# Optimization experiments

Hardware: AMD Instinct MI355X
Metric: run time of the kernel (lower is better)

The kernel has to match this reference:

```python
import jax, jax.numpy as jnp
import numpy as np

EPS = 1e-5  # torch InstanceNorm2d default eps

def instance_norm(x):
    # per-sample, per-channel normalization over spatial dims (affine=False)
    m = jnp.mean(x, axis=(2, 3), keepdims=True)
    v = jnp.var(x, axis=(2, 3), keepdims=True)
    return (x - m) * jax.lax.rsqrt(v + EPS)

def conv2d(x, w, b, stride, pad):
    y = jax.lax.conv_general_dilated(
        x, w, (stride, stride), [(pad, pad), (pad, pad)],
        dimension_numbers=('NCHW', 'OIHW', 'NCHW'))
    return y + b[None, :, None, None]

def res_block(x, w1, b1, w2, b2):
    out = conv2d(jax.nn.relu(instance_norm(x)), w1, b1, 1, 1)
    out = conv2d(jax.nn.relu(instance_norm(out)), w2, b2, 1, 1)
    return out + x

def res_block_strided(x, w1, b1, w2, b2, ws, bs):
    out = conv2d(jax.nn.relu(instance_norm(x)), w1, b1, 2, 1)
    out = conv2d(jax.nn.relu(instance_norm(out)), w2, b2, 1, 1)
    return out + conv2d(x, ws, bs, 2, 0)  # 1x1 strided skip projection

def setup_inputs() -> dict:
    key = jax.random.key(0)
    ks = jax.random.split(key, 12)
    B, N, C, H, W = 64, 1, 3, 256, 256
    TEXT, EMB, F, HEADS = 256, 512, 32, 5
    FH, FW = H // 16, W // 16  # 16, 16
    def rn(k, shape, scale=0.05):
        return jax.random.normal(k, shape, dtype=jnp.float32) * scale
    z = lambda *s: jnp.zeros(s, jnp.float32)
    return {
        'x': jax.random.normal(ks[0], (B, N, C, H, W), jnp.float32),
        'text_vector': jax.random.normal(ks[1], (B, TEXT), jnp.float32),
        'conv1_w': rn(ks[2], (F, C, 7, 7)),
        'conv1_b': z(F),
        'rbs_w1': rn(ks[3], (3, F, F, 3, 3)),  # 3 strided resblocks
        'rbs_b1': z(3, F),
        'rbs_w2': rn(ks[4], (3, F, F, 3, 3)),
        'rbs_b2': z(3, F),
        'rbs_ws': rn(ks[5], (3, F, F, 1, 1)),
        'rbs_bs': z(3, F),
        'rb_w1': rn(ks[6], (2, F, F, 3, 3)),  # 2 plain resblocks
        'rb_b1': z(2, F),
        'rb_w2': rn(ks[7], (2, F, F, 3, 3)),
        'rb_b2': z(2, F),
        'attn_w': rn(ks[8], (HEADS, FH * FW, TEXT)),  # torch Linear [out,in] per head
        'attn_b': z(HEADS, FH * FW),
        'final_w': rn(ks[9], (EMB, FH * FW * HEADS)),
        'final_b': z(EMB),
    }

def reference(x, text_vector, conv1_w, conv1_b, rbs_w1, rbs_b1, rbs_w2, rbs_b2,
              rbs_ws, rbs_bs, rb_w1, rb_b1, rb_w2, rb_b2, attn_w, attn_b,
              final_w, final_b):
    B, N, C, H, W = x.shape
    feat = x.reshape(B, N * C, H, W)
    feat = instance_norm(feat)
    feat = conv2d(feat, conv1_w, conv1_b, 2, 3)
    # block1 = strided + plain; block2 = strided + plain; block3 = strided
    feat = res_block_strided(feat, rbs_w1[0], rbs_b1[0], rbs_w2[0], rbs_b2[0], rbs_ws[0], rbs_bs[0])
    feat = res_block(feat, rb_w1[0], rb_b1[0], rb_w2[0], rb_b2[0])
    feat = res_block_strided(feat, rbs_w1[1], rbs_b1[1], rbs_w2[1], rbs_b2[1], rbs_ws[1], rbs_bs[1])
    feat = res_block(feat, rb_w1[1], rb_b1[1], rb_w2[1], rb_b2[1])
    feat = res_block_strided(feat, rbs_w1[2], rbs_b1[2], rbs_w2[2], rbs_b2[2], rbs_ws[2], rbs_bs[2])
    # feat: [B, 32, FH, FW]
    HEADS = attn_w.shape[0]
    FH, FW = feat.shape[2], feat.shape[3]
    # sigmoid-gated spatial attention logits per head: [B, HEADS, FH, FW]
    a = jax.nn.sigmoid(jnp.einsum('bt,hot->bho', text_vector, attn_w) + attn_b[None])
    a = a.reshape(B, HEADS, FH, FW)
    # channel scores: spatial sum of gate * feature -> [B, HEADS, C]
    scores = jnp.einsum('bhij,bcij->bhc', a, feat)
    probs = jax.nn.softmax(scores, axis=-1)  # old F.softmax over channel dim
    # weighted channel sum -> per-head attention map [B, HEADS, FH, FW]
    amaps = jnp.einsum('bhc,bcij->bhij', probs, feat)
    out = amaps.reshape(B, -1) @ final_w.T + final_b
    return out
```

## Files before the change

kernel.cpp:

```cpp
#include <hip/hip_runtime.h>
#include <cstdint>
#include <cstddef>

#define INORM_EPS 1e-5f

typedef _Float16 f16;
typedef f16 f16x8 __attribute__((ext_vector_type(8)));
typedef f16 f16x4 __attribute__((ext_vector_type(4)));
typedef float f32x4 __attribute__((ext_vector_type(4)));

__global__ __launch_bounds__(256) void prep(
    const float* __restrict__ rbs_w1, const float* __restrict__ rbs_w2,
    const float* __restrict__ rb_w1, const float* __restrict__ rb_w2,
    const float* __restrict__ rbs_ws, const float* __restrict__ conv1_w,
    float2* __restrict__ SP, f16* __restrict__ wp3, f16* __restrict__ wp1,
    f16* __restrict__ wp7) {
  int i = blockIdx.x * 256 + threadIdx.x;
  if (i < 20672) { SP[i] = make_float2(0.f, 0.f); return; }
  i -= 20672;
  if (i < 92160) {
    int mat = i / 9216, r = i % 9216;
    int p = r >> 10, f = (r >> 9) & 1, l = (r >> 3) & 63, j = r & 7;
    int co = f * 16 + (l & 15), ci = (l >> 4) * 8 + j;
    const float* src; int m;
    if (mat < 3) { src = rbs_w1; m = mat; }
    else if (mat < 6) { src = rbs_w2; m = mat - 3; }
    else if (mat < 8) { src = rb_w1; m = mat - 6; }
    else { src = rb_w2; m = mat - 8; }
    wp3[i] = (f16)src[m * 9216 + co * 288 + ci * 9 + p];
    return;
  }
  i -= 92160;
  if (i < 3072) {
    int mat = i / 1024, r = i % 1024;
    int f = r >> 9, l = (r >> 3) & 63, j = r & 7;
    wp1[i] = (f16)rbs_ws[mat * 1024 + (f * 16 + (l & 15)) * 32 + (l >> 4) * 8 + j];
    return;
  }
  i -= 3072;
  if (i >= 7168) return;
  int ky = i >> 10, f = (i >> 9) & 1, l = (i >> 3) & 63, j = i & 7;
  int k = (l >> 4) * 8 + j, kx = k >> 2, ci = k & 3;
  float v = 0.f;
  if (kx < 7 && ci < 3) v = conv1_w[(f * 16 + (l & 15)) * 147 + ci * 49 + ky * 7 + kx];
  wp7[i] = (f16)v;
}

__global__ __launch_bounds__(256) void stats_raw(const float* __restrict__ in,
                                                 float2* __restrict__ st, int HW) {
  const int map = blockIdx.x >> 3, chunk = blockIdx.x & 7;
  const int n4 = HW >> 5;
  const float4* p = (const float4*)(in + (size_t)map * HW + (size_t)chunk * (HW >> 3));
  float s = 0.f, ss = 0.f;
  for (int i = threadIdx.x; i < n4; i += 256) {
    float4 v = p[i];
    s += v.x + v.y + v.z + v.w;
    ss += v.x * v.x + v.y * v.y + v.z * v.z + v.w * v.w;
  }
  __shared__ float r0[256], r1[256];
  r0[threadIdx.x] = s;
  r1[threadIdx.x] = ss;
  __syncthreads();
  for (int off = 128; off > 0; off >>= 1) {
    if ((int)threadIdx.x < off) {
      r0[threadIdx.x] += r0[threadIdx.x + off];
      r1[threadIdx.x] += r1[threadIdx.x + off];
    }
    __syncthreads();
  }
  if (threadIdx.x == 0) {
    atomicAdd(&st[map].x, r0[0]);
    atomicAdd(&st[map].y, r1[0]);
  }
}

__global__ __launch_bounds__(256) void packx(const float* __restrict__ x,
                                             const float2* __restrict__ SPx,
                                             f16* __restrict__ xP) {
  int u = blockIdx.x * 256 + threadIdx.x;
  if (u >= 262 * 262) return;
  int b = blockIdx.z;
  int r = u / 262, c = u % 262;
  f16x4 out;
  out[0] = (f16)0; out[1] = (f16)0; out[2] = (f16)0; out[3] = (f16)0;
  if (r >= 3 && r < 259 && c >= 3 && c < 259) {
    int ir = r - 3, ic = c - 3;
#pragma unroll
    for (int ci = 0; ci < 3; ci++) {
      float2 s = SPx[b * 3 + ci];
      float mean = s.x * (1.f / 65536.f);
      float rstd = rsqrtf(s.y * (1.f / 65536.f) - mean * mean + INORM_EPS);
      out[ci] = (f16)((x[((size_t)b * 3 + ci) * 65536 + ir * 256 + ic] - mean) * rstd);
    }
  }
  *(f16x4*)(xP + ((size_t)b * 68644 + u) * 4) = out;
}

template <int W, int SKIP>
__global__ __launch_bounds__(256) void conv3r(
    const f16* __restrict__ Rin, const float2* __restrict__ SPin, float inv_hw,
    const f16* __restrict__ wp, const float* __restrict__ bias,
    const float* __restrict__ bias2, const f16* __restrict__ skip,
    const f16* __restrict__ wps, f16* __restrict__ Rout,
    float2* __restrict__ ostats) {
  constexpr int TPR = W / 16;
  constexpr int RPB = 8;
  constexpr int LEN = (RPB * TPR) / 4;
  const int t = threadIdx.x, w = t >> 6, l = t & 63;
  const int n = l & 15, q = l >> 4;
  const int b = blockIdx.z;
  const int tx = w % TPR;
  const int y0 = blockIdx.x * RPB + (w / TPR) * LEN;
  const int x = (tx << 4) + n;
  const f16* Rb = Rin + (size_t)b * W * W * 32;

  f16x8 sc, sh;
#pragma unroll
  for (int j = 0; j < 8; j++) {
    float2 s = SPin[b * 32 + q * 8 + j];
    float mean = s.x * inv_hw;
    float rstd = rsqrtf(s.y * inv_hw - mean * mean + INORM_EPS);
    sc[j] = (f16)rstd;
    sh[j] = (f16)(-mean * rstd);
  }

  f16x8 wf[18];
#pragma unroll
  for (int i = 0; i < 18; i++) wf[i] = *(const f16x8*)(wp + i * 512 + l * 8);
  f16x8 wsf0, wsf1;
  if (SKIP == 2) {
    wsf0 = *(const f16x8*)(wps + l * 8);
    wsf1 = *(const f16x8*)(wps + 512 + l * 8);
  }
  float b0 = bias[n], b1 = bias[16 + n];
  if (SKIP == 2) { b0 += bias2[n]; b1 += bias2[16 + n]; }

  f16* ro = Rout + (size_t)b * W * W * 32;
  const f16* sb = skip ? skip + (size_t)b * (SKIP == 2 ? 4 : 1) * W * W * 32 : nullptr;

  bool okc[3];
#pragma unroll
  for (int kx = 0; kx < 3; kx++) okc[kx] = (unsigned)(x + kx - 1) < (unsigned)W;

  auto rowload = [&](int gy, f16x8* dst) {
    int gyc = min(max(gy, 0), W - 1);
#pragma unroll
    for (int kx = 0; kx < 3; kx++) {
      int gxc = min(max(x + kx - 1, 0), W - 1);
      dst[kx] = *(const f16x8*)(Rb + ((size_t)gyc * W + gxc) * 32 + q * 8);
    }
  };
  auto rownorm = [&](int gy, const f16x8* src, f16x8* dst) {
    bool okr = (unsigned)gy < (unsigned)W;
#pragma unroll
    for (int kx = 0; kx < 3; kx++) {
      f16x8 v = src[kx] * sc + sh;
#pragma unroll
      for (int e = 0; e < 8; e++) v[e] = v[e] > (f16)0 ? v[e] : (f16)0;
      f16x8 z = {};
      dst[kx] = (okr && okc[kx]) ? v : z;
    }
  };

  float sm0 = 0.f, sq0 = 0.f, sm1 = 0.f, sq1 = 0.f;
  f16x8 win[9];
  f16x8 tmp[3], pf[3];
#pragma unroll
  for (int jj = 0; jj < 3; jj++) {
    rowload(y0 + jj - 1, tmp);
    rownorm(y0 + jj - 1, tmp, &win[jj * 3]);
  }

#pragma unroll
  for (int i = 0; i < LEN; i++) {
    int y = y0 + i;
    if (i + 1 < LEN) rowload(y0 + i + 2, pf);
    f32x4 acc0 = {0.f, 0.f, 0.f, 0.f}, acc1 = {0.f, 0.f, 0.f, 0.f};
#pragma unroll
    for (int ky = 0; ky < 3; ky++) {
      int slot = (i + ky) % 3;
#pragma unroll
      for (int kx = 0; kx < 3; kx++) {
        f16x8 a = win[slot * 3 + kx];
        acc0 = __builtin_amdgcn_mfma_f32_16x16x32_f16(a, wf[2 * (ky * 3 + kx)], acc0, 0, 0, 0);
        acc1 = __builtin_amdgcn_mfma_f32_16x16x32_f16(a, wf[2 * (ky * 3 + kx) + 1], acc1, 0, 0, 0);
      }
    }
    if (SKIP == 2) {
      const int Ws = 2 * W;
      f16x8 as = *(const f16x8*)(sb + ((size_t)(2 * y) * Ws + 2 * x) * 32 + q * 8);
      acc0 = __builtin_amdgcn_mfma_f32_16x16x32_f16(as, wsf0, acc0, 0, 0, 0);
      acc1 = __builtin_amdgcn_mfma_f32_16x16x32_f16(as, wsf1, acc1, 0, 0, 0);
    }
#pragma unroll
    for (int r = 0; r < 4; r++) {
      size_t px = (size_t)y * W + (tx << 4) + q * 4 + r;
      float v0 = acc0[r] + b0;
      float v1 = acc1[r] + b1;
      if (SKIP == 1) {
        v0 += (float)sb[px * 32 + n];
        v1 += (float)sb[px * 32 + 16 + n];
      }
      ro[px * 32 + n] = (f16)v0;
      ro[px * 32 + 16 + n] = (f16)v1;
      sm0 += v0; sq0 += v0 * v0;
      sm1 += v1; sq1 += v1 * v1;
    }
    if (i + 1 < LEN) rownorm(y0 + i + 2, pf, &win[(i % 3) * 3]);
  }
  if (ostats) {
    sm0 += __shfl_xor(sm0, 16); sm0 += __shfl_xor(sm0, 32);
    sq0 += __shfl_xor(sq0, 16); sq0 += __shfl_xor(sq0, 32);
    sm1 += __shfl_xor(sm1, 16); sm1 += __shfl_xor(sm1, 32);
    sq1 += __shfl_xor(sq1, 16); sq1 += __shfl_xor(sq1, 32);
    if (l < 16) {
      atomicAdd(&ostats[b * 32 + n].x, sm0);
      atomicAdd(&ostats[b * 32 + n].y, sq0);
      atomicAdd(&ostats[b * 32 + 16 + n].x, sm1);
      atomicAdd(&ostats[b * 32 + 16 + n].y, sq1);
    }
  }
}

template <int WIN, int STRIDE, int SKIP>
__global__ __launch_bounds__(256) void conv3n(
    const f16* __restrict__ Rin, const float2* __restrict__ SPin, float inv_hw,
    const f16* __restrict__ wp, const float* __restrict__ bias,
    const float* __restrict__ bias2, const f16* __restrict__ skip,
    const f16* __restrict__ wps, f16* __restrict__ Rout,
    float2* __restrict__ ostats) {
  constexpr int WOUT = WIN / STRIDE;
  constexpr int TPR = WOUT / 16;
  constexpr int RPB = (WOUT >= 32) ? 4 : 8;
  constexpr int UNITS = TPR * RPB;
  constexpr int U = UNITS / 4;
  const int t = threadIdx.x, w = t >> 6, l = t & 63;
  const int n = l & 15, q = l >> 4;
  const int b = blockIdx.z;
  const int yb = blockIdx.x * RPB;
  const f16* Rb = Rin + (size_t)b * WIN * WIN * 32;

  f16x8 sc, sh;
#pragma unroll
  for (int j = 0; j < 8; j++) {
    float2 s = SPin[b * 32 + q * 8 + j];
    float mean = s.x * inv_hw;
    float rstd = rsqrtf(s.y * inv_hw - mean * mean + INORM_EPS);
    sc[j] = (f16)rstd;
    sh[j] = (f16)(-mean * rstd);
  }

  f16x8 wf[18];
#pragma unroll
  for (int i = 0; i < 18; i++) wf[i] = *(const f16x8*)(wp + i * 512 + l * 8);
  f16x8 wsf0, wsf1;
  if (SKIP == 2) {
    wsf0 = *(const f16x8*)(wps + l * 8);
    wsf1 = *(const f16x8*)(wps + 512 + l * 8);
  }
  float b0 = bias[n], b1 = bias[16 + n];
  if (SKIP == 2) { b0 += bias2[n]; b1 += bias2[16 + n]; }

  f16* ro = Rout + (size_t)b * WOUT * WOUT * 32;
  const f16* sb = skip ? skip + (size_t)b * (SKIP == 2 ? 4 : 1) * WOUT * WOUT * 32 : nullptr;

  auto load_u = [&](int u, f16x8* a) {
    int ty = u / TPR, tx = u % TPR;
    int y = yb + ty;
#pragma unroll
    for (int kx = 0; kx < 3; kx++) {
      int gx = STRIDE * ((tx << 4) + n) + kx - 1;
      int gxc = min(max(gx, 0), WIN - 1);
#pragma unroll
      for (int ky = 0; ky < 3; ky++) {
        int gy = STRIDE * y + ky - 1;
        int gyc = min(max(gy, 0), WIN - 1);
        a[ky * 3 + kx] = *(const f16x8*)(Rb + ((size_t)gyc * WIN + gxc) * 32 + q * 8);
      }
    }
  };
  auto norm_u = [&](int u, f16x8* a) {
    int ty = u / TPR, tx = u % TPR;
    int y = yb + ty;
#pragma unroll
    for (int kx = 0; kx < 3; kx++) {
      int gx = STRIDE * ((tx << 4) + n) + kx - 1;
      bool okx = (unsigned)gx < (unsigned)WIN;
#pragma unroll
      for (int ky = 0; ky < 3; ky++) {
        int gy = STRIDE * y + ky - 1;
        bool ok = okx && ((unsigned)gy < (unsigned)WIN);
        f16x8 v = a[ky * 3 + kx] * sc + sh;
#pragma unroll
        for (int e = 0; e < 8; e++) v[e] = v[e] > (f16)0 ? v[e] : (f16)0;
        f16x8 z = {};
        a[ky * 3 + kx] = ok ? v : z;
      }
    }
  };

  float sm0 = 0.f, sq0 = 0.f, sm1 = 0.f, sq1 = 0.f;
  f16x8 araw[9], anxt[9];
  load_u(w, araw);
#pragma unroll
  for (int i = 0; i < U; i++) {
    int u = w + 4 * i;
    if (i + 1 < U) load_u(u + 4, anxt);
    norm_u(u, araw);
    int ty = u / TPR, tx = u % TPR;
    int y = yb + ty, x0 = tx << 4;
    f32x4 acc0 = {0.f, 0.f, 0.f, 0.f}, acc1 = {0.f, 0.f, 0.f, 0.f};
#pragma unroll
    for (int p = 0; p < 9; p++) {
      acc0 = __builtin_amdgcn_mfma_f32_16x16x32_f16(araw[p], wf[2 * p], acc0, 0, 0, 0);
      acc1 = __builtin_amdgcn_mfma_f32_16x16x32_f16(araw[p], wf[2 * p + 1], acc1, 0, 0, 0);
    }
    if (SKIP == 2) {
      const int Ws = 2 * WOUT;
      f16x8 as = *(const f16x8*)(sb + ((size_t)(2 * y) * Ws + 2 * (x0 + n)) * 32 + q * 8);
      acc0 = __builtin_amdgcn_mfma_f32_16x16x32_f16(as, wsf0, acc0, 0, 0, 0);
      acc1 = __builtin_amdgcn_mfma_f32_16x16x32_f16(as, wsf1, acc1, 0, 0, 0);
    }
#pragma unroll
    for (int r = 0; r < 4; r++) {
      size_t px = (size_t)y * WOUT + x0 + q * 4 + r;
      float v0 = acc0[r] + b0;
      float v1 = acc1[r] + b1;
      if (SKIP == 1) {
        v0 += (float)sb[px * 32 + n];
        v1 += (float)sb[px * 32 + 16 + n];
      }
      ro[px * 32 + n] = (f16)v0;
      ro[px * 32 + 16 + n] = (f16)v1;
      sm0 += v0; sq0 += v0 * v0;
      sm1 += v1; sq1 += v1 * v1;
    }
#pragma unroll
    for (int p = 0; p < 9; p++) araw[p] = anxt[p];
  }
  if (ostats) {
    sm0 += __shfl_xor(sm0, 16); sm0 += __shfl_xor(sm0, 32);
    sq0 += __shfl_xor(sq0, 16); sq0 += __shfl_xor(sq0, 32);
    sm1 += __shfl_xor(sm1, 16); sm1 += __shfl_xor(sm1, 32);
    sq1 += __shfl_xor(sq1, 16); sq1 += __shfl_xor(sq1, 32);
    if (l < 16) {
      atomicAdd(&ostats[b * 32 + n].x, sm0);
      atomicAdd(&ostats[b * 32 + n].y, sq0);
      atomicAdd(&ostats[b * 32 + 16 + n].x, sm1);
      atomicAdd(&ostats[b * 32 + 16 + n].y, sq1);
    }
  }
}

__global__ __launch_bounds__(256) void conv7(
    const f16* __restrict__ xP, const f16* __restrict__ wp,
    const float* __restrict__ bias, f16* __restrict__ Rout,
    float2* __restrict__ ostats) {
  const int t = threadIdx.x, w = t >> 6, l = t & 63;
  const int n = l & 15, q = l >> 4;
  const int b = blockIdx.z;
  const int yb = blockIdx.x * 8;
  const f16* Xb = xP + (size_t)b * 68644 * 4;
  f16x8 wf[14];
#pragma unroll
  for (int i = 0; i < 14; i++) wf[i] = *(const f16x8*)(wp + i * 512 + l * 8);
  float b0 = bias[n], b1 = bias[16 + n];
  float sm0 = 0.f, sq0 = 0.f, sm1 = 0.f, sq1 = 0.f;
  f16* ro = Rout + (size_t)b * 16384 * 32;

#pragma unroll
  for (int seg = 0; seg < 2; seg++) {
    const int tx = w + seg * 4;
    const int x0 = tx * 16;
    const f16* base = Xb + (size_t)(2 * (x0 + n) + 2 * q) * 4;
    f16x8 win[7];
#pragma unroll
    for (int j = 0; j < 7; j++)
      win[j] = *(const f16x8*)(base + (size_t)(2 * yb + j) * 1048);
    f16x8 pf0, pf1;
#pragma unroll
    for (int i = 0; i < 8; i++) {
      if (i < 7) {
        pf0 = *(const f16x8*)(base + (size_t)(2 * yb + 2 * i + 7) * 1048);
        pf1 = *(const f16x8*)(base + (size_t)(2 * yb + 2 * i + 8) * 1048);
      }
      int y = yb + i;
      f32x4 acc0 = {0.f, 0.f, 0.f, 0.f}, acc1 = {0.f, 0.f, 0.f, 0.f};
#pragma unroll
      for (int ky = 0; ky < 7; ky++) {
        f16x8 a = win[(2 * i + ky) % 7];
        acc0 = __builtin_amdgcn_mfma_f32_16x16x32_f16(a, wf[2 * ky], acc0, 0, 0, 0);
        acc1 = __builtin_amdgcn_mfma_f32_16x16x32_f16(a, wf[2 * ky + 1], acc1, 0, 0, 0);
      }
#pragma unroll
      for (int r = 0; r < 4; r++) {
        size_t px = (size_t)y * 128 + x0 + q * 4 + r;
        float v0 = acc0[r] + b0;
        float v1 = acc1[r] + b1;
        ro[px * 32 + n] = (f16)v0;
        ro[px * 32 + 16 + n] = (f16)v1;
        sm0 += v0; sq0 += v0 * v0;
        sm1 += v1; sq1 += v1 * v1;
      }
      if (i < 7) {
        win[(2 * i) % 7] = pf0;
        win[(2 * i + 1) % 7] = pf1;
      }
    }
  }
  sm0 += __shfl_xor(sm0, 16); sm0 += __shfl_xor(sm0, 32);
  sq0 += __shfl_xor(sq0, 16); sq0 += __shfl_xor(sq0, 32);
  sm1 += __shfl_xor(sm1, 16); sm1 += __shfl_xor(sm1, 32);
  sq1 += __shfl_xor(sq1, 16); sq1 += __shfl_xor(sq1, 32);
  if (l < 16) {
    atomicAdd(&ostats[b * 32 + n].x, sm0);
    atomicAdd(&ostats[b * 32 + n].y, sq0);
    atomicAdd(&ostats[b * 32 + 16 + n].x, sm1);
    atomicAdd(&ostats[b * 32 + 16 + n].y, sq1);
  }
}

__global__ __launch_bounds__(256) void gates_kernel(
    const float* __restrict__ text, const float* __restrict__ attn_w,
    const float* __restrict__ attn_b, float* __restrict__ G) {
  __shared__ float s_text[64 * 257];
  __shared__ float s_w[16 * 256];
  const int t = threadIdx.x, wv = t >> 6, lane = t & 63;
  const int o0 = blockIdx.x * 16;
  for (int d = t; d < 16384; d += 256) {
    int b = d >> 8, k = d & 255;
    s_text[b * 257 + k] = text[d];
  }
  for (int d = t; d < 4096; d += 256) s_w[d] = attn_w[(size_t)o0 * 256 + d];
  __syncthreads();
  float acc[4];
#pragma unroll
  for (int j = 0; j < 4; j++) acc[j] = attn_b[o0 + wv * 4 + j];
  for (int k = 0; k < 256; k++) {
    float tv = s_text[lane * 257 + k];
#pragma unroll
    for (int j = 0; j < 4; j++) acc[j] = fmaf(s_w[(wv * 4 + j) * 256 + k], tv, acc[j]);
  }
#pragma unroll
  for (int j = 0; j < 4; j++) {
    int o = o0 + wv * 4 + j;
    G[o * 64 + lane] = 1.f / (1.f + __expf(-acc[j]));
  }
}

__global__ __launch_bounds__(256) void scores_kernel(
    const f16* __restrict__ feat, const float* __restrict__ G,
    float* __restrict__ amapT) {
  __shared__ float s_feat[256 * 33];
  __shared__ float s_gate[1280];
  __shared__ float s_scores[5 * 32];
  __shared__ float s_probs[5 * 32];
  const int b = blockIdx.x;
  const int t = threadIdx.x;

  for (int i = t; i < 8192; i += 256)
    s_feat[(i >> 5) * 33 + (i & 31)] = (float)feat[(size_t)b * 8192 + i];
  for (int i = t; i < 1280; i += 256) s_gate[i] = G[i * 64 + b];
  __syncthreads();

  if (t < 160) {
    int h = t >> 5, c = t & 31;
    float acc = 0.f;
    for (int ij = 0; ij < 256; ij++) acc += s_gate[h * 256 + ij] * s_feat[ij * 33 + c];
    s_scores[t] = acc;
  }
  __syncthreads();

  if (t < 5) {
    float mx = -1e30f;
    for (int c = 0; c < 32; c++) mx = fmaxf(mx, s_scores[t * 32 + c]);
    float sum = 0.f;
    for (int c = 0; c < 32; c++) {
      float e = __expf(s_scores[t * 32 + c] - mx);
      s_probs[t * 32 + c] = e;
      sum += e;
    }
    float inv = 1.f / sum;
    for (int c = 0; c < 32; c++) s_probs[t * 32 + c] *= inv;
  }
  __syncthreads();

  for (int h = 0; h < 5; h++) {
    float acc = 0.f;
    for (int c = 0; c < 32; c++) acc += s_probs[h * 32 + c] * s_feat[t * 33 + c];
    amapT[(h * 256 + t) * 64 + b] = acc;
  }
}

__global__ __launch_bounds__(256) void final_kernel(
    const float* __restrict__ amapT, const float* __restrict__ final_w,
    const float* __restrict__ final_b, float* __restrict__ out) {
  __shared__ float s_w[4 * 1280];
  __shared__ float s_red[4][4][64];
  const int t = threadIdx.x, wv = t >> 6, lane = t & 63;
  const int e0 = blockIdx.x * 4;
  for (int d = t; d < 5120; d += 256) s_w[d] = final_w[(size_t)e0 * 1280 + d];
  __syncthreads();
  const int k0 = wv * 320;
  float acc[4] = {0.f, 0.f, 0.f, 0.f};
  for (int k = k0; k < k0 + 320; k++) {
    float av = amapT[k * 64 + lane];
#pragma unroll
    for (int e = 0; e < 4; e++) acc[e] = fmaf(s_w[e * 1280 + k], av, acc[e]);
  }
#pragma unroll
  for (int e = 0; e < 4; e++) s_red[wv][e][lane] = acc[e];
  __syncthreads();
  if (wv == 0) {
#pragma unroll
    for (int e = 0; e < 4; e++) {
      float v = s_red[0][e][lane] + s_red[1][e][lane] + s_red[2][e][lane] +
                s_red[3][e][lane] + final_b[e0 + e];
      out[(size_t)lane * 512 + e0 + e] = v;
    }
  }
}

extern "C" void kernel_launch(void* const* d_in, const int* in_sizes, int n_in,
                              void* d_out, int out_size, void* d_ws, size_t ws_size,
                              hipStream_t stream) {
  (void)in_sizes; (void)n_in; (void)out_size; (void)ws_size;
  const float* x       = (const float*)d_in[0];
  const float* text    = (const float*)d_in[1];
  const float* conv1_w = (const float*)d_in[2];
  const float* conv1_b = (const float*)d_in[3];
  const float* rbs_w1  = (const float*)d_in[4];
  const float* rbs_b1  = (const float*)d_in[5];
  const float* rbs_w2  = (const float*)d_in[6];
  const float* rbs_b2  = (const float*)d_in[7];
  const float* rbs_ws  = (const float*)d_in[8];
  const float* rbs_bs  = (const float*)d_in[9];
  const float* rb_w1   = (const float*)d_in[10];
  const float* rb_b1   = (const float*)d_in[11];
  const float* rb_w2   = (const float*)d_in[12];
  const float* rb_b2   = (const float*)d_in[13];
  const float* attn_w  = (const float*)d_in[14];
  const float* attn_b  = (const float*)d_in[15];
  const float* final_w = (const float*)d_in[16];
  const float* final_b = (const float*)d_in[17];
  float* out = (float*)d_out;

  char* wsb = (char*)d_ws;
  f16*   xP   = (f16*)(wsb + 0);
  f16*   R128 = (f16*)(wsb + 35145728);
  f16*   R64a = (f16*)(wsb + 102254592);
  f16*   R64b = (f16*)(wsb + 119031808);
  f16*   R64c = (f16*)(wsb + 135809024);
  f16*   R32a = (f16*)(wsb + 152586240);
  f16*   R32b = (f16*)(wsb + 156780544);
  f16*   R32c = (f16*)(wsb + 160974848);
  f16*   R16a = (f16*)(wsb + 165169152);
  f16*   R16b = (f16*)(wsb + 166217728);
  float2* SP  = (float2*)(wsb + 167266304);
  float2* SPx = (float2*)(wsb + 167430144);
  f16*   wp3  = (f16*)(wsb + 167431680);
  f16*   wp1  = (f16*)(wsb + 167616000);
  f16*   wp7  = (f16*)(wsb + 167622144);
  float* G     = (float*)(wsb + 167636480);
  float* amapT = (float*)(wsb + 167964160);
  float2* SP0 = SP + 0 * 2048;
  float2* SP1 = SP + 1 * 2048;
  float2* SP2 = SP + 2 * 2048;
  float2* SP3 = SP + 3 * 2048;
  float2* SP4 = SP + 4 * 2048;
  float2* SP5 = SP + 5 * 2048;
  float2* SP6 = SP + 6 * 2048;
  float2* SP7 = SP + 7 * 2048;
  float2* SP8 = SP + 8 * 2048;
  float2* SP9 = SP + 9 * 2048;

  prep<<<481, 256, 0, stream>>>(rbs_w1, rbs_w2, rb_w1, rb_w2, rbs_ws, conv1_w,
                                SP, wp3, wp1, wp7);
  stats_raw<<<1536, 256, 0, stream>>>(x, SPx, 65536);
  packx<<<dim3(269, 1, 64), 256, 0, stream>>>(x, SPx, xP);

  conv7<<<dim3(16, 1, 64), 256, 0, stream>>>(xP, wp7, conv1_b, R128, SP0);

  conv3n<128, 2, 0><<<dim3(16, 1, 64), 256, 0, stream>>>(
      R128, SP0, 1.f / 16384.f, wp3, rbs_b1, nullptr, nullptr, nullptr, R64a, SP1);
  conv3r<64, 2><<<dim3(8, 1, 64), 256, 0, stream>>>(
      R64a, SP1, 1.f / 4096.f, wp3 + 3 * 9216, rbs_b2, rbs_bs, R128, wp1, R64b, SP2);

  conv3r<64, 0><<<dim3(8, 1, 64), 256, 0, stream>>>(
      R64b, SP2, 1.f / 4096.f, wp3 + 6 * 9216, rb_b1, nullptr, nullptr, nullptr, R64c, SP3);
  conv3r<64, 1><<<dim3(8, 1, 64), 256, 0, stream>>>(
      R64c, SP3, 1.f / 4096.f, wp3 + 8 * 9216, rb_b2, nullptr, R64b, nullptr, R64a, SP4);

  conv3n<64, 2, 0><<<dim3(8, 1, 64), 256, 0, stream>>>(
      R64a, SP4, 1.f / 4096.f, wp3 + 1 * 9216, rbs_b1 + 32, nullptr, nullptr, nullptr, R32a, SP5);
  conv3r<32, 2><<<dim3(4, 1, 64), 256, 0, stream>>>(
      R32a, SP5, 1.f / 1024.f, wp3 + 4 * 9216, rbs_b2 + 32, rbs_bs + 32, R64a, wp1 + 1024, R32b, SP6);

  conv3r<32, 0><<<dim3(4, 1, 64), 256, 0, stream>>>(
      R32b, SP6, 1.f / 1024.f, wp3 + 7 * 9216, rb_b1 + 32, nullptr, nullptr, nullptr, R32c, SP7);
  conv3r<32, 1><<<dim3(4, 1, 64), 256, 0, stream>>>(
      R32c, SP7, 1.f / 1024.f, wp3 + 9 * 9216, rb_b2 + 32, nullptr, R32b, nullptr, R32a, SP8);

  conv3n<32, 2, 0><<<dim3(2, 1, 64), 256, 0, stream>>>(
      R32a, SP8, 1.f / 1024.f, wp3 + 2 * 9216, rbs_b1 + 64, nullptr, nullptr, nullptr, R16a, SP9);
  conv3n<16, 1, 2><<<dim3(2, 1, 64), 256, 0, stream>>>(
      R16a, SP9, 1.f / 256.f, wp3 + 5 * 9216, rbs_b2 + 64, rbs_bs + 64, R32a, wp1 + 2048, R16b, nullptr);

  gates_kernel<<<80, 256, 0, stream>>>(text, attn_w, attn_b, G);
  scores_kernel<<<64, 256, 0, stream>>>(R16b, G, amapT);
  final_kernel<<<128, 256, 0, stream>>>(amapT, final_w, final_b, out);
}
```

Before: 331.2 us.

## Stage conv weights in LDS, raise occupancy bounds, halve conv3r rows per block

Conv kernels now copy the packed filter weights into shared memory once per block and read MFMA B-operands from LDS instead of holding 18 f16x8 weight vectors in registers. Launch bounds ask for 4 blocks per SM to cut register pressure and raise occupancy. conv3r processes fewer rows per block, so its grid doubles for more parallelism. The cost is extra LDS reads per MFMA, a block-wide sync, and more redundant weight loads and halo rows across the larger number of blocks.

After: 341.0 us. 3.0% more time.

```diff
diff --git a/kernel.cpp b/kernel.cpp
--- a/kernel.cpp
+++ b/kernel.cpp
@@ -97,15 +97,17 @@
 }
 
 template <int W, int SKIP>
-__global__ __launch_bounds__(256) void conv3r(
+__global__ __launch_bounds__(256, 4) void conv3r(
     const f16* __restrict__ Rin, const float2* __restrict__ SPin, float inv_hw,
     const f16* __restrict__ wp, const float* __restrict__ bias,
     const float* __restrict__ bias2, const f16* __restrict__ skip,
     const f16* __restrict__ wps, f16* __restrict__ Rout,
     float2* __restrict__ ostats) {
   constexpr int TPR = W / 16;
-  constexpr int RPB = 8;
-  constexpr int LEN = (RPB * TPR) / 4;
+  constexpr int LEN = (W == 64) ? 4 : 2;
+  constexpr int RPB = (4 / TPR) * LEN;
+  __shared__ f16 s_w[9216];
+  __shared__ f16 s_ws[1024];
   const int t = threadIdx.x, w = t >> 6, l = t & 63;
   const int n = l & 15, q = l >> 4;
   const int b = blockIdx.z;
@@ -114,6 +116,9 @@
   const int x = (tx << 4) + n;
   const f16* Rb = Rin + (size_t)b * W * W * 32;
 
+  for (int d = t; d < 1152; d += 256) ((uint4*)s_w)[d] = ((const uint4*)wp)[d];
+  if (SKIP == 2 && t < 128) ((uint4*)s_ws)[t] = ((const uint4*)wps)[t];
+
   f16x8 sc, sh;
 #pragma unroll
   for (int j = 0; j < 8; j++) {
@@ -123,17 +128,9 @@
     sc[j] = (f16)rstd;
     sh[j] = (f16)(-mean * rstd);
   }
-
-  f16x8 wf[18];
-#pragma unroll
-  for (int i = 0; i < 18; i++) wf[i] = *(const f16x8*)(wp + i * 512 + l * 8);
-  f16x8 wsf0, wsf1;
-  if (SKIP == 2) {
-    wsf0 = *(const f16x8*)(wps + l * 8);
-    wsf1 = *(const f16x8*)(wps + 512 + l * 8);
-  }
   float b0 = bias[n], b1 = bias[16 + n];
   if (SKIP == 2) { b0 += bias2[n]; b1 += bias2[16 + n]; }
+  __syncthreads();
 
   f16* ro = Rout + (size_t)b * W * W * 32;
   const f16* sb = skip ? skip + (size_t)b * (SKIP == 2 ? 4 : 1) * W * W * 32 : nullptr;
@@ -182,15 +179,16 @@
 #pragma unroll
       for (int kx = 0; kx < 3; kx++) {
         f16x8 a = win[slot * 3 + kx];
-        acc0 = __builtin_amdgcn_mfma_f32_16x16x32_f16(a, wf[2 * (ky * 3 + kx)], acc0, 0, 0, 0);
-        acc1 = __builtin_amdgcn_mfma_f32_16x16x32_f16(a, wf[2 * (ky * 3 + kx) + 1], acc1, 0, 0, 0);
+        const f16* wb = s_w + (ky * 3 + kx) * 1024 + l * 8;
+        acc0 = __builtin_amdgcn_mfma_f32_16x16x32_f16(a, *(const f16x8*)wb, acc0, 0, 0, 0);
+        acc1 = __builtin_amdgcn_mfma_f32_16x16x32_f16(a, *(const f16x8*)(wb + 512), acc1, 0, 0, 0);
       }
     }
     if (SKIP == 2) {
       const int Ws = 2 * W;
       f16x8 as = *(const f16x8*)(sb + ((size_t)(2 * y) * Ws + 2 * x) * 32 + q * 8);
-      acc0 = __builtin_amdgcn_mfma_f32_16x16x32_f16(as, wsf0, acc0, 0, 0, 0);
-      acc1 = __builtin_amdgcn_mfma_f32_16x16x32_f16(as, wsf1, acc1, 0, 0, 0);
+      acc0 = __builtin_amdgcn_mfma_f32_16x16x32_f16(as, *(const f16x8*)(s_ws + l * 8), acc0, 0, 0, 0);
+      acc1 = __builtin_amdgcn_mfma_f32_16x16x32_f16(as, *(const f16x8*)(s_ws + 512 + l * 8), acc1, 0, 0, 0);
     }
 #pragma unroll
     for (int r = 0; r < 4; r++) {
@@ -223,7 +221,7 @@
 }
 
 template <int WIN, int STRIDE, int SKIP>
-__global__ __launch_bounds__(256) void conv3n(
+__global__ __launch_bounds__(256, 4) void conv3n(
     const f16* __restrict__ Rin, const float2* __restrict__ SPin, float inv_hw,
     const f16* __restrict__ wp, const float* __restrict__ bias,
     const float* __restrict__ bias2, const f16* __restrict__ skip,
@@ -234,11 +232,16 @@
   constexpr int RPB = (WOUT >= 32) ? 4 : 8;
   constexpr int UNITS = TPR * RPB;
   constexpr int U = UNITS / 4;
+  __shared__ f16 s_w[9216];
+  __shared__ f16 s_ws[1024];
   const int t = threadIdx.x, w = t >> 6, l = t & 63;
   const int n = l & 15, q = l >> 4;
   const int b = blockIdx.z;
   const int yb = blockIdx.x * RPB;
   const f16* Rb = Rin + (size_t)b * WIN * WIN * 32;
+
+  for (int d = t; d < 1152; d += 256) ((uint4*)s_w)[d] = ((const uint4*)wp)[d];
+  if (SKIP == 2 && t < 128) ((uint4*)s_ws)[t] = ((const uint4*)wps)[t];
 
   f16x8 sc, sh;
 #pragma unroll
@@ -249,17 +252,9 @@
     sc[j] = (f16)rstd;
     sh[j] = (f16)(-mean * rstd);
   }
-
-  f16x8 wf[18];
-#pragma unroll
-  for (int i = 0; i < 18; i++) wf[i] = *(const f16x8*)(wp + i * 512 + l * 8);
-  f16x8 wsf0, wsf1;
-  if (SKIP == 2) {
-    wsf0 = *(const f16x8*)(wps + l * 8);
-    wsf1 = *(const f16x8*)(wps + 512 + l * 8);
-  }
   float b0 = bias[n], b1 = bias[16 + n];
   if (SKIP == 2) { b0 += bias2[n]; b1 += bias2[16 + n]; }
+  __syncthreads();
 
   f16* ro = Rout + (size_t)b * WOUT * WOUT * 32;
   const f16* sb = skip ? skip + (size_t)b * (SKIP == 2 ? 4 : 1) * WOUT * WOUT * 32 : nullptr;
@@ -312,14 +307,15 @@
     f32x4 acc0 = {0.f, 0.f, 0.f, 0.f}, acc1 = {0.f, 0.f, 0.f, 0.f};
 #pragma unroll
     for (int p = 0; p < 9; p++) {
-      acc0 = __builtin_amdgcn_mfma_f32_16x16x32_f16(araw[p], wf[2 * p], acc0, 0, 0, 0);
-      acc1 = __builtin_amdgcn_mfma_f32_16x16x32_f16(araw[p], wf[2 * p + 1], acc1, 0, 0, 0);
+      const f16* wb = s_w + p * 1024 + l * 8;
+      acc0 = __builtin_amdgcn_mfma_f32_16x16x32_f16(araw[p], *(const f16x8*)wb, acc0, 0, 0, 0);
+      acc1 = __builtin_amdgcn_mfma_f32_16x16x32_f16(araw[p], *(const f16x8*)(wb + 512), acc1, 0, 0, 0);
     }
     if (SKIP == 2) {
       const int Ws = 2 * WOUT;
       f16x8 as = *(const f16x8*)(sb + ((size_t)(2 * y) * Ws + 2 * (x0 + n)) * 32 + q * 8);
-      acc0 = __builtin_amdgcn_mfma_f32_16x16x32_f16(as, wsf0, acc0, 0, 0, 0);
-      acc1 = __builtin_amdgcn_mfma_f32_16x16x32_f16(as, wsf1, acc1, 0, 0, 0);
+      acc0 = __builtin_amdgcn_mfma_f32_16x16x32_f16(as, *(const f16x8*)(s_ws + l * 8), acc0, 0, 0, 0);
+      acc1 = __builtin_amdgcn_mfma_f32_16x16x32_f16(as, *(const f16x8*)(s_ws + 512 + l * 8), acc1, 0, 0, 0);
     }
 #pragma unroll
     for (int r = 0; r < 4; r++) {
@@ -352,19 +348,19 @@
   }
 }
 
-__global__ __launch_bounds__(256) void conv7(
+__global__ __launch_bounds__(256, 4) void conv7(
     const f16* __restrict__ xP, const f16* __restrict__ wp,
     const float* __restrict__ bias, f16* __restrict__ Rout,
     float2* __restrict__ ostats) {
+  __shared__ f16 s_w[7168];
   const int t = threadIdx.x, w = t >> 6, l = t & 63;
   const int n = l & 15, q = l >> 4;
   const int b = blockIdx.z;
   const int yb = blockIdx.x * 8;
   const f16* Xb = xP + (size_t)b * 68644 * 4;
-  f16x8 wf[14];
-#pragma unroll
-  for (int i = 0; i < 14; i++) wf[i] = *(const f16x8*)(wp + i * 512 + l * 8);
+  for (int d = t; d < 896; d += 256) ((uint4*)s_w)[d] = ((const uint4*)wp)[d];
   float b0 = bias[n], b1 = bias[16 + n];
+  __syncthreads();
   float sm0 = 0.f, sq0 = 0.f, sm1 = 0.f, sq1 = 0.f;
   f16* ro = Rout + (size_t)b * 16384 * 32;
 
@@ -389,8 +385,9 @@
 #pragma unroll
       for (int ky = 0; ky < 7; ky++) {
         f16x8 a = win[(2 * i + ky) % 7];
-        acc0 = __builtin_amdgcn_mfma_f32_16x16x32_f16(a, wf[2 * ky], acc0, 0, 0, 0);
-        acc1 = __builtin_amdgcn_mfma_f32_16x16x32_f16(a, wf[2 * ky + 1], acc1, 0, 0, 0);
+        const f16* wb = s_w + 2 * ky * 512 + l * 8;
+        acc0 = __builtin_amdgcn_mfma_f32_16x16x32_f16(a, *(const f16x8*)wb, acc0, 0, 0, 0);
+        acc1 = __builtin_amdgcn_mfma_f32_16x16x32_f16(a, *(const f16x8*)(wb + 512), acc1, 0, 0, 0);
       }
 #pragma unroll
       for (int r = 0; r < 4; r++) {
@@ -583,22 +580,22 @@
 
   conv3n<128, 2, 0><<<dim3(16, 1, 64), 256, 0, stream>>>(
       R128, SP0, 1.f / 16384.f, wp3, rbs_b1, nullptr, nullptr, nullptr, R64a, SP1);
-  conv3r<64, 2><<<dim3(8, 1, 64), 256, 0, stream>>>(
+  conv3r<64, 2><<<dim3(16, 1, 64), 256, 0, stream>>>(
       R64a, SP1, 1.f / 4096.f, wp3 + 3 * 9216, rbs_b2, rbs_bs, R128, wp1, R64b, SP2);
 
-  conv3r<64, 0><<<dim3(8, 1, 64), 256, 0, stream>>>(
+  conv3r<64, 0><<<dim3(16, 1, 64), 256, 0, stream>>>(
       R64b, SP2, 1.f / 4096.f, wp3 + 6 * 9216, rb_b1, nullptr, nullptr, nullptr, R64c, SP3);
-  conv3r<64, 1><<<dim3(8, 1, 64), 256, 0, stream>>>(
+  conv3r<64, 1><<<dim3(16, 1, 64), 256, 0, stream>>>(
       R64c, SP3, 1.f / 4096.f, wp3 + 8 * 9216, rb_b2, nullptr, R64b, nullptr, R64a, SP4);
 
   conv3n<64, 2, 0><<<dim3(8, 1, 64), 256, 0, stream>>>(
       R64a, SP4, 1.f / 4096.f, wp3 + 1 * 9216, rbs_b1 + 32, nullptr, nullptr, nullptr, R32a, SP5);
-  conv3r<32, 2><<<dim3(4, 1, 64), 256, 0, stream>>>(
+  conv3r<32, 2><<<dim3(8, 1, 64), 256, 0, stream>>>(
       R32a, SP5, 1.f / 1024.f, wp3 + 4 * 9216, rbs_b2 + 32, rbs_bs + 32, R64a, wp1 + 1024, R32b, SP6);
 
-  conv3r<32, 0><<<dim3(4, 1, 64), 256, 0, stream>>>(
+  conv3r<32, 0><<<dim3(8, 1, 64), 256, 0, stream>>>(
       R32b, SP6, 1.f / 1024.f, wp3 + 7 * 9216, rb_b1 + 32, nullptr, nullptr, nullptr, R32c, SP7);
-  conv3r<32, 1><<<dim3(4, 1, 64), 256, 0, stream>>>(
+  conv3r<32, 1><<<dim3(8, 1, 64), 256, 0, stream>>>(
       R32c, SP7, 1.f / 1024.f, wp3 + 9 * 9216, rb_b2 + 32, nullptr, R32b, nullptr, R32a, SP8);
 
   conv3n<32, 2, 0><<<dim3(2, 1, 64), 256, 0, stream>>>(
```

## Compute strided 1x1 skip projection inside first strided conv from its centre tap

Applied to the files above, without the earlier changes.

The 1x1 stride-2 skip projection moves out of the second conv of each strided resblock and into the first strided conv. That conv already holds the raw centre-tap input (the same strided pixel the projection reads), so it issues two extra MFMAs and writes the projected result plus bias to a new fp16 buffer. The second conv then does a plain residual add from that buffer instead of a strided gather from the full-resolution input. This trades a sparse, poorly coalesced gather for an extra contiguous write and read of a half-resolution tensor, and adds one fp16 rounding of the projection.

Measured after the change: 337.0 us. Within noise of the previous version (+1.7%).

```diff
diff --git a/kernel.cpp b/kernel.cpp
--- a/kernel.cpp
+++ b/kernel.cpp
@@ -100,8 +100,7 @@
 __global__ __launch_bounds__(256) void conv3r(
     const f16* __restrict__ Rin, const float2* __restrict__ SPin, float inv_hw,
     const f16* __restrict__ wp, const float* __restrict__ bias,
-    const float* __restrict__ bias2, const f16* __restrict__ skip,
-    const f16* __restrict__ wps, f16* __restrict__ Rout,
+    const f16* __restrict__ skip, f16* __restrict__ Rout,
     float2* __restrict__ ostats) {
   constexpr int TPR = W / 16;
   constexpr int RPB = 8;
@@ -127,16 +126,10 @@
   f16x8 wf[18];
 #pragma unroll
   for (int i = 0; i < 18; i++) wf[i] = *(const f16x8*)(wp + i * 512 + l * 8);
-  f16x8 wsf0, wsf1;
-  if (SKIP == 2) {
-    wsf0 = *(const f16x8*)(wps + l * 8);
-    wsf1 = *(const f16x8*)(wps + 512 + l * 8);
-  }
   float b0 = bias[n], b1 = bias[16 + n];
-  if (SKIP == 2) { b0 += bias2[n]; b1 += bias2[16 + n]; }
 
   f16* ro = Rout + (size_t)b * W * W * 32;
-  const f16* sb = skip ? skip + (size_t)b * (SKIP == 2 ? 4 : 1) * W * W * 32 : nullptr;
+  const f16* sb = skip ? skip + (size_t)b * W * W * 32 : nullptr;
 
   bool okc[3];
 #pragma unroll
@@ -185,12 +178,6 @@
         acc0 = __builtin_amdgcn_mfma_f32_16x16x32_f16(a, wf[2 * (ky * 3 + kx)], acc0, 0, 0, 0);
         acc1 = __builtin_amdgcn_mfma_f32_16x16x32_f16(a, wf[2 * (ky * 3 + kx) + 1], acc1, 0, 0, 0);
       }
-    }
-    if (SKIP == 2) {
-      const int Ws = 2 * W;
-      f16x8 as = *(const f16x8*)(sb + ((size_t)(2 * y) * Ws + 2 * x) * 32 + q * 8);
-      acc0 = __builtin_amdgcn_mfma_f32_16x16x32_f16(as, wsf0, acc0, 0, 0, 0);
-      acc1 = __builtin_amdgcn_mfma_f32_16x16x32_f16(as, wsf1, acc1, 0, 0, 0);
     }
 #pragma unroll
     for (int r = 0; r < 4; r++) {
@@ -222,13 +209,13 @@
   }
 }
 
-template <int WIN, int STRIDE, int SKIP>
+template <int WIN, int STRIDE, int SKIP, int PROJ>
 __global__ __launch_bounds__(256) void conv3n(
     const f16* __restrict__ Rin, const float2* __restrict__ SPin, float inv_hw,
     const f16* __restrict__ wp, const float* __restrict__ bias,
     const float* __restrict__ bias2, const f16* __restrict__ skip,
-    const f16* __restrict__ wps, f16* __restrict__ Rout,
-    float2* __restrict__ ostats) {
+    const f16* __restrict__ wps, f16* __restrict__ proj,
+    f16* __restrict__ Rout, float2* __restrict__ ostats) {
   constexpr int WOUT = WIN / STRIDE;
   constexpr int TPR = WOUT / 16;
   constexpr int RPB = (WOUT >= 32) ? 4 : 8;
@@ -253,16 +240,19 @@
   f16x8 wf[18];
 #pragma unroll
   for (int i = 0; i < 18; i++) wf[i] = *(const f16x8*)(wp + i * 512 + l * 8);
-  f16x8 wsf0, wsf1;
-  if (SKIP == 2) {
-    wsf0 = *(const f16x8*)(wps + l * 8);
-    wsf1 = *(const f16x8*)(wps + 512 + l * 8);
+  f16x8 wpf0, wpf1;
+  float pb0 = 0.f, pb1 = 0.f;
+  if (PROJ) {
+    wpf0 = *(const f16x8*)(wps + l * 8);
+    wpf1 = *(const f16x8*)(wps + 512 + l * 8);
+    pb0 = bias2[n];
+    pb1 = bias2[16 + n];
   }
   float b0 = bias[n], b1 = bias[16 + n];
-  if (SKIP == 2) { b0 += bias2[n]; b1 += bias2[16 + n]; }
 
   f16* ro = Rout + (size_t)b * WOUT * WOUT * 32;
-  const f16* sb = skip ? skip + (size_t)b * (SKIP == 2 ? 4 : 1) * WOUT * WOUT * 32 : nullptr;
+  f16* po = PROJ ? proj + (size_t)b * WOUT * WOUT * 32 : nullptr;
+  const f16* sb = skip ? skip + (size_t)b * WOUT * WOUT * 32 : nullptr;
 
   auto load_u = [&](int u, f16x8* a) {
     int ty = u / TPR, tx = u % TPR;
@@ -306,6 +296,7 @@
   for (int i = 0; i < U; i++) {
     int u = w + 4 * i;
     if (i + 1 < U) load_u(u + 4, anxt);
+    f16x8 rawc = araw[4];
     norm_u(u, araw);
     int ty = u / TPR, tx = u % TPR;
     int y = yb + ty, x0 = tx << 4;
@@ -315,11 +306,10 @@
       acc0 = __builtin_amdgcn_mfma_f32_16x16x32_f16(araw[p], wf[2 * p], acc0, 0, 0, 0);
       acc1 = __builtin_amdgcn_mfma_f32_16x16x32_f16(araw[p], wf[2 * p + 1], acc1, 0, 0, 0);
     }
-    if (SKIP == 2) {
-      const int Ws = 2 * WOUT;
-      f16x8 as = *(const f16x8*)(sb + ((size_t)(2 * y) * Ws + 2 * (x0 + n)) * 32 + q * 8);
-      acc0 = __builtin_amdgcn_mfma_f32_16x16x32_f16(as, wsf0, acc0, 0, 0, 0);
-      acc1 = __builtin_amdgcn_mfma_f32_16x16x32_f16(as, wsf1, acc1, 0, 0, 0);
+    f32x4 pc0 = {0.f, 0.f, 0.f, 0.f}, pc1 = {0.f, 0.f, 0.f, 0.f};
+    if (PROJ) {
+      pc0 = __builtin_amdgcn_mfma_f32_16x16x32_f16(rawc, wpf0, pc0, 0, 0, 0);
+      pc1 = __builtin_amdgcn_mfma_f32_16x16x32_f16(rawc, wpf1, pc1, 0, 0, 0);
     }
 #pragma unroll
     for (int r = 0; r < 4; r++) {
@@ -332,6 +322,10 @@
       }
       ro[px * 32 + n] = (f16)v0;
       ro[px * 32 + 16 + n] = (f16)v1;
+      if (PROJ) {
+        po[px * 32 + n] = (f16)(pc0[r] + pb0);
+        po[px * 32 + 16 + n] = (f16)(pc1[r] + pb1);
+      }
       sm0 += v0; sq0 += v0 * v0;
       sm1 += v1; sq1 += v1 * v1;
     }
@@ -563,6 +557,9 @@
   f16*   wp7  = (f16*)(wsb + 167622144);
   float* G     = (float*)(wsb + 167636480);
   float* amapT = (float*)(wsb + 167964160);
+  f16*   Pr64 = (f16*)(wsb + 168291840);
+  f16*   Pr32 = (f16*)(wsb + 185069056);
+  f16*   Pr16 = (f16*)(wsb + 189263360);
   float2* SP0 = SP + 0 * 2048;
   float2* SP1 = SP + 1 * 2048;
   float2* SP2 = SP + 2 * 2048;
@@ -581,30 +578,33 @@
 
   conv7<<<dim3(16, 1, 64), 256, 0, stream>>>(xP, wp7, conv1_b, R128, SP0);
 
-  conv3n<128, 2, 0><<<dim3(16, 1, 64), 256, 0, stream>>>(
-      R128, SP0, 1.f / 16384.f, wp3, rbs_b1, nullptr, nullptr, nullptr, R64a, SP1);
-  conv3r<64, 2><<<dim3(8, 1, 64), 256, 0, stream>>>(
-      R64a, SP1, 1.f / 4096.f, wp3 + 3 * 9216, rbs_b2, rbs_bs, R128, wp1, R64b, SP2);
+  conv3n<128, 2, 0, 1><<<dim3(16, 1, 64), 256, 0, stream>>>(
+      R128, SP0, 1.f / 16384.f, wp3, rbs_b1, rbs_bs, nullptr, wp1, Pr64, R64a, SP1);
+  conv3r<64, 1><<<dim3(8, 1, 64), 256, 0, stream>>>(
+      R64a, SP1, 1.f / 4096.f, wp3 + 3 * 9216, rbs_b2, Pr64, R64b, SP2);
 
   conv3r<64, 0><<<dim3(8, 1, 64), 256, 0, stream>>>(
-      R64b, SP2, 1.f / 4096.f, wp3 + 6 * 9216, rb_b1, nullptr, nullptr, nullptr, R64c, SP3);
+      R64b, SP2, 1.f / 4096.f, wp3 + 6 * 9216, rb_b1, nullptr, R64c, SP3);
   conv3r<64, 1><<<dim3(8, 1, 64), 256, 0, stream>>>(
-      R64c, SP3, 1.f / 4096.f, wp3 + 8 * 9216, rb_b2, nullptr, R64b, nullptr, R64a, SP4);
-
-  conv3n<64, 2, 0><<<dim3(8, 1, 64), 256, 0, stream>>>(
-      R64a, SP4, 1.f / 4096.f, wp3 + 1 * 9216, rbs_b1 + 32, nullptr, nullptr, nullptr, R32a, SP5);
-  conv3r<32, 2><<<dim3(4, 1, 64), 256, 0, stream>>>(
-      R32a, SP5, 1.f / 1024.f, wp3 + 4 * 9216, rbs_b2 + 32, rbs_bs + 32, R64a, wp1 + 1024, R32b, SP6);
+      R64c, SP3, 1.f / 4096.f, wp3 + 8 * 9216, rb_b2, R64b, R64a, SP4);
+
+  conv3n<64, 2, 0, 1><<<dim3(8, 1, 64), 256, 0, stream>>>(
+      R64a, SP4, 1.f / 4096.f, wp3 + 1 * 9216, rbs_b1 + 32, rbs_bs + 32,
+      nullptr, wp1 + 1024, Pr32, R32a, SP5);
+  conv3r<32, 1><<<dim3(4, 1, 64), 256, 0, stream>>>(
+      R32a, SP5, 1.f / 1024.f, wp3 + 4 * 9216, rbs_b2 + 32, Pr32, R32b, SP6);
 
   conv3r<32, 0><<<dim3(4, 1, 64), 256, 0, stream>>>(
-      R32b, SP6, 1.f / 1024.f, wp3 + 7 * 9216, rb_b1 + 32, nullptr, nullptr, nullptr, R32c, SP7);
+      R32b, SP6, 1.f / 1024.f, wp3 + 7 * 9216, rb_b1 + 32, nullptr, R32c, SP7);
   conv3r<32, 1><<<dim3(4, 1, 64), 256, 0, stream>>>(
-      R32c, SP7, 1.f / 1024.f, wp3 + 9 * 9216, rb_b2 + 32, nullptr, R32b, nullptr, R32a, SP8);
-
-  conv3n<32, 2, 0><<<dim3(2, 1, 64), 256, 0, stream>>>(
-      R32a, SP8, 1.f / 1024.f, wp3 + 2 * 9216, rbs_b1 + 64, nullptr, nullptr, nullptr, R16a, SP9);
-  conv3n<16, 1, 2><<<dim3(2, 1, 64), 256, 0, stream>>>(
-      R16a, SP9, 1.f / 256.f, wp3 + 5 * 9216, rbs_b2 + 64, rbs_bs + 64, R32a, wp1 + 2048, R16b, nullptr);
+      R32c, SP7, 1.f / 1024.f, wp3 + 9 * 9216, rb_b2 + 32, R32b, R32a, SP8);
+
+  conv3n<32, 2, 0, 1><<<dim3(2, 1, 64), 256, 0, stream>>>(
+      R32a, SP8, 1.f / 1024.f, wp3 + 2 * 9216, rbs_b1 + 64, rbs_bs + 64,
+      nullptr, wp1 + 2048, Pr16, R16a, SP9);
+  conv3n<16, 1, 1, 0><<<dim3(2, 1, 64), 256, 0, stream>>>(
+      R16a, SP9, 1.f / 256.f, wp3 + 5 * 9216, rbs_b2 + 64, nullptr,
+      Pr16, nullptr, nullptr, R16b, nullptr);
 
   gates_kernel<<<80, 256, 0, stream>>>(text, attn_w, attn_b, G);
   scores_kernel<<<64, 256, 0, stream>>>(R16b, G, amapT);
```
